# Performance work log

Hardware: AMD Instinct MI355X
Metric: run time of the kernel (lower is better)

## Reference

```python
import jax, jax.numpy as jnp
import numpy as np
from jax import lax

B, H, W = 256, 26, 4
LAT, QOUT = 64, 1024
K, D, Z = 4, 32, 64   # num_flows, num_ortho_vecs, z_size
STEPS = 100
BN_EPS = 1e-5


def setup_inputs():
    ks = iter(jax.random.split(jax.random.key(0), 80))
    def rn(shape, s=0.05):
        return jax.random.normal(next(ks), shape, jnp.float32) * s
    z1 = lambda n: jnp.zeros((n,), jnp.float32)
    o1 = lambda n: jnp.ones((n,), jnp.float32)
    return {
        "x": jax.random.normal(next(ks), (B, 1, H, W), jnp.float32),
        "eps": jax.random.normal(next(ks), (B, LAT), jnp.float32),
        "cw1": rn((32, 1, 3, 4)), "cb1": z1(32), "g1": o1(32), "be1": z1(32),
        "cw2": rn((16, 32, 5, 1)), "cb2": z1(16), "g2": o1(16), "be2": z1(16),
        "cw3": rn((8, 16, 7, 1)), "cb3": z1(8), "g3": o1(8), "be3": z1(8),
        "d1_w": rn((112, QOUT)), "d1_b": z1(QOUT), "bn1_g": o1(QOUT), "bn1_b": z1(QOUT),
        "mu_w": rn((QOUT, LAT)), "mu_b": z1(LAT),
        "lv_w": rn((QOUT, LAT)), "lv_b": z1(LAT),
        "ad_w": rn((QOUT, K * D * D)), "ad_b": z1(K * D * D),
        "adg1_w": rn((QOUT, K * D)), "adg1_b": z1(K * D),
        "adg2_w": rn((QOUT, K * D)), "adg2_b": z1(K * D),
        "aq_w": rn((QOUT, K * Z * D)), "aq_b": rn((K * Z * D,), 0.05),
        "ab_w": rn((QOUT, K * D)), "ab_b": z1(K * D),
        "d3_w": rn((LAT, QOUT)), "d3_b": z1(QOUT), "bn3_g": o1(QOUT), "bn3_b": z1(QOUT),
        "d4_w": rn((QOUT, 112)), "d4_b": z1(112), "bn4_g": o1(112), "bn4_b": z1(112),
        "tw1": rn((8, 16, 7, 1)), "tb1": z1(16), "tg1": o1(16), "tbe1": z1(16),
        "tw2": rn((16, 32, 5, 1)), "tb2": z1(32), "tg2": o1(32), "tbe2": z1(32),
        "tw3": rn((32, 1, 3, 4)), "tb3": z1(1),
    }


def _conv(x, w, b):
    y = lax.conv_general_dilated(x, w, (1, 1), 'VALID',
                                 dimension_numbers=('NCHW', 'OIHW', 'NCHW'))
    return y + b[None, :, None, None]


def _tconv(x, w, b):
    # torch ConvTranspose2d weight layout (in, out, kH, kW) == OIHW of the
    # forward conv being transposed -> transpose_kernel=True matches torch.
    y = lax.conv_transpose(x, w, (1, 1), 'VALID',
                           dimension_numbers=('NCHW', 'OIHW', 'NCHW'),
                           transpose_kernel=True)
    return y + b[None, :, None, None]


def _bn2d(x, g, b):  # BatchNorm2d, training mode (biased batch stats)
    m = x.mean((0, 2, 3), keepdims=True)
    v = ((x - m) ** 2).mean((0, 2, 3), keepdims=True)
    return (x - m) * lax.rsqrt(v + BN_EPS) * g[None, :, None, None] + b[None, :, None, None]


def _bn1d(x, g, b):  # BatchNorm1d, training mode
    m = x.mean(0)
    v = ((x - m) ** 2).mean(0)
    return (x - m) * lax.rsqrt(v + BN_EPS) * g + b


def reference(x, eps, cw1, cb1, g1, be1, cw2, cb2, g2, be2, cw3, cb3, g3, be3,
              d1_w, d1_b, bn1_g, bn1_b, mu_w, mu_b, lv_w, lv_b,
              ad_w, ad_b, adg1_w, adg1_b, adg2_w, adg2_b, aq_w, aq_b, ab_w, ab_b,
              d3_w, d3_b, bn3_g, bn3_b, d4_w, d4_b, bn4_g, bn4_b,
              tw1, tb1, tg1, tbe1, tw2, tb2, tg2, tbe2, tw3, tb3):
    # ---- encoder CNN ----
    h = jax.nn.relu(_bn2d(_conv(x, cw1, cb1), g1, be1))
    h = jax.nn.relu(_bn2d(_conv(h, cw2, cb2), g2, be2))
    h = jax.nn.relu(_bn2d(_conv(h, cw3, cb3), g3, be3))   # (B,8,14,1)
    out = h.reshape(B, -1)                                 # (B,112)
    out = jax.nn.relu(_bn1d(out @ d1_w + d1_b, bn1_g, bn1_b))
    mean = out @ mu_w + mu_b
    logvar = out @ lv_w + lv_b
    # ---- amortized flow parameters ----
    full_d = (out @ ad_w + ad_b).reshape(B, D, D, K)
    diag1 = jnp.tanh(out @ adg1_w + adg1_b).reshape(B, D, K)
    diag2 = jnp.tanh(out @ adg2_w + adg2_b).reshape(B, D, K)
    triu = jnp.triu(jnp.ones((D, D), x.dtype), 1)[None, :, :, None]
    di = jnp.arange(D)
    r1 = (full_d * triu).at[:, di, di, :].set(diag1)
    r2 = (jnp.transpose(full_d, (0, 2, 1, 3)) * triu).at[:, di, di, :].set(diag2)
    q = out @ aq_w + aq_b                                  # (B, K*Z*D)
    bflow = (out @ ab_w + ab_b).reshape(B, 1, D, K)
    # ---- Bjorck orthogonalization (100 fixed-point steps) ----
    qn = q.reshape(B * K, Z * D)
    qn = qn / jnp.linalg.norm(qn, axis=1, keepdims=True)
    amat = qn.reshape(B * K, Z, D)
    eye = jnp.eye(D, dtype=x.dtype)
    @jax.checkpoint
    def step(a, _):
        gram = jnp.einsum('nzd,nze->nde', a, a)            # a^T a, (N,D,D)
        a = jnp.einsum('nzd,nde->nze', a, eye + 0.5 * (eye - gram))
        return a, None
    amat, _ = lax.scan(step, amat, None, length=STEPS)
    q_ortho = amat.reshape(B, K, Z, D).transpose(1, 0, 2, 3)  # (K,B,Z,D)
    # ---- reparameterize + Sylvester flows ----
    z0 = mean + eps * jnp.exp(0.5 * logvar)
    z = z0
    ldj = jnp.zeros((B,), x.dtype)
    for k in range(K):
        r1k, r2k, qk, bk = r1[..., k], r2[..., k], q_ortho[k], bflow[..., k]
        qr2 = jnp.einsum('bzd,bed->bze', qk, r2k)          # q @ r2^T (B,Z,D)
        qr1 = jnp.einsum('bzd,bde->bze', qk, r1k)          # q @ r1   (B,Z,D)
        r2qzb = jnp.einsum('bz,bzd->bd', z, qr2)[:, None, :] + bk  # (B,1,D)
        z = jnp.einsum('bod,bzd->boz', jnp.tanh(r2qzb), qr1)[:, 0, :] + z
        dr1 = r1k[:, di, di]
        dr2 = r2k[:, di, di]
        diag_j = (1.0 - jnp.tanh(r2qzb) ** 2)[:, 0, :] * (dr1 * dr2) + 1.0
        ldj = ldj + jnp.log(jnp.abs(diag_j)).sum(-1)
    # ---- decoder ----
    d = jax.nn.relu(_bn1d(z @ d3_w + d3_b, bn3_g, bn3_b))
    d = jax.nn.relu(_bn1d(d @ d4_w + d4_b, bn4_g, bn4_b))
    d = d.reshape(B, 8, 14, 1)
    d = jax.nn.relu(_bn2d(_tconv(d, tw1, tb1), tg1, tbe1))
    d = jax.nn.relu(_bn2d(_tconv(d, tw2, tb2), tg2, tbe2))
    x_dec = _tconv(d, tw3, tb3)
    return (x_dec, mean, logvar, ldj, z0, z)
```

## Files before the change

### kernel.cpp

```cpp
#include <hip/hip_runtime.h>
#include <math.h>

#define NS_STEPS 30

typedef __attribute__((ext_vector_type(8))) _Float16 half8;
typedef __attribute__((ext_vector_type(4))) _Float16 half4v;
typedef __attribute__((ext_vector_type(8))) short short8;
typedef __attribute__((ext_vector_type(4))) float floatx4;

static __device__ inline unsigned short f2bf(float f) {
  union { float f; unsigned u; } v; v.f = f;
  unsigned r = v.u + 0x7fffu + ((v.u >> 16) & 1u);
  return (unsigned short)(r >> 16);
}
static __device__ inline float bf2f(unsigned short h) {
  union { unsigned u; float f; } v; v.u = ((unsigned)h) << 16;
  return v.f;
}

__global__ __launch_bounds__(256) void conv1_k(const float* __restrict__ x,
    const float* __restrict__ w, const float* __restrict__ bias,
    float* __restrict__ out) {
  __shared__ float ws[384];
  int tid = threadIdx.x;
  for (int i = tid; i < 384; i += 256) ws[i] = w[i];
  __syncthreads();
  int idx = blockIdx.x * 256 + tid;
  if (idx >= 196608) return;
  int b = idx / 768, r = idx % 768;
  int c = r / 24, h = r % 24;
  const float* xb = x + b * 104 + h * 4;
  const float* wc = ws + c * 12;
  float acc = bias[c];
  #pragma unroll
  for (int kh = 0; kh < 3; kh++) {
    #pragma unroll
    for (int kw = 0; kw < 4; kw++)
      acc += xb[kh * 4 + kw] * wc[kh * 4 + kw];
  }
  out[idx] = acc;
}

__global__ __launch_bounds__(256) void conv2_k(const float* __restrict__ in,
    const float* __restrict__ w, const float* __restrict__ bias,
    float* __restrict__ out) {
  __shared__ float ws[2560];
  int tid = threadIdx.x;
  for (int i = tid; i < 2560; i += 256) ws[i] = w[i];
  __syncthreads();
  int idx = blockIdx.x * 256 + tid;
  if (idx >= 81920) return;
  int b = idx / 320, r = idx % 320;
  int c = r / 20, h = r % 20;
  const float* ib = in + b * 768 + h;
  const float* wc = ws + c * 160;
  float acc = bias[c];
  for (int i = 0; i < 32; i++) {
    #pragma unroll
    for (int kh = 0; kh < 5; kh++)
      acc += ib[i * 24 + kh] * wc[i * 5 + kh];
  }
  out[idx] = acc;
}

__global__ __launch_bounds__(256) void conv3_k(const float* __restrict__ in,
    const float* __restrict__ w, const float* __restrict__ bias,
    float* __restrict__ out) {
  __shared__ float ws[896];
  int tid = threadIdx.x;
  for (int i = tid; i < 896; i += 256) ws[i] = w[i];
  __syncthreads();
  int idx = blockIdx.x * 256 + tid;
  if (idx >= 28672) return;
  int b = idx / 112, r = idx % 112;
  int c = r / 14, h = r % 14;
  const float* ib = in + b * 320 + h;
  const float* wc = ws + c * 112;
  float acc = bias[c];
  for (int i = 0; i < 16; i++) {
    #pragma unroll
    for (int kh = 0; kh < 7; kh++)
      acc += ib[i * 20 + kh] * wc[i * 7 + kh];
  }
  out[idx] = acc;
}

__global__ __launch_bounds__(256) void tconv1_k(const float* __restrict__ in,
    const float* __restrict__ w, const float* __restrict__ bias,
    float* __restrict__ out) {
  __shared__ float ws[896];
  int tid = threadIdx.x;
  for (int i = tid; i < 896; i += 256) ws[i] = w[i];
  __syncthreads();
  int idx = blockIdx.x * 256 + tid;
  if (idx >= 81920) return;
  int b = idx / 320, r = idx % 320;
  int c = r / 20, s = r % 20;
  float acc = bias[c];
  for (int o = 0; o < 8; o++) {
    #pragma unroll
    for (int kh = 0; kh < 7; kh++) {
      int hs = s - kh;
      if (hs >= 0 && hs < 14)
        acc += in[b * 112 + o * 14 + hs] * ws[o * 112 + c * 7 + kh];
    }
  }
  out[idx] = acc;
}

__global__ __launch_bounds__(256) void tconv2_k(const float* __restrict__ in,
    const float* __restrict__ w, const float* __restrict__ bias,
    float* __restrict__ out) {
  __shared__ float ws[2560];
  int tid = threadIdx.x;
  for (int i = tid; i < 2560; i += 256) ws[i] = w[i];
  __syncthreads();
  int idx = blockIdx.x * 256 + tid;
  if (idx >= 196608) return;
  int b = idx / 768, r = idx % 768;
  int c = r / 24, s = r % 24;
  float acc = bias[c];
  for (int o = 0; o < 16; o++) {
    #pragma unroll
    for (int kh = 0; kh < 5; kh++) {
      int hs = s - kh;
      if (hs >= 0 && hs < 20)
        acc += in[b * 320 + o * 20 + hs] * ws[o * 160 + c * 5 + kh];
    }
  }
  out[idx] = acc;
}

__global__ __launch_bounds__(256) void tconv3_k(const float* __restrict__ in,
    const float* __restrict__ w, const float* __restrict__ bias,
    float* __restrict__ out) {
  __shared__ float ws[384];
  int tid = threadIdx.x;
  for (int i = tid; i < 384; i += 256) ws[i] = w[i];
  __syncthreads();
  int idx = blockIdx.x * 256 + tid;
  if (idx >= 26624) return;
  int b = idx / 104, r = idx % 104;
  int sh = r / 4, sw = r % 4;
  float acc = bias[0];
  for (int o = 0; o < 32; o++) {
    #pragma unroll
    for (int kh = 0; kh < 3; kh++) {
      int hs = sh - kh;
      if (hs >= 0 && hs < 24)
        acc += in[b * 768 + o * 24 + hs] * ws[o * 12 + kh * 4 + sw];
    }
  }
  out[idx] = acc;
}

__global__ __launch_bounds__(256) void bn2d_k(float* __restrict__ x,
    const float* __restrict__ g, const float* __restrict__ be,
    int C, int HW) {
  __shared__ float rs[256], rs2[256];
  int c = blockIdx.x, tid = threadIdx.x;
  int total = 256 * HW;
  float s = 0.f, s2 = 0.f;
  for (int i = tid; i < total; i += 256) {
    int b = i / HW, j = i - b * HW;
    float v = x[(b * C + c) * HW + j];
    s += v; s2 += v * v;
  }
  rs[tid] = s; rs2[tid] = s2;
  __syncthreads();
  for (int off = 128; off > 0; off >>= 1) {
    if (tid < off) { rs[tid] += rs[tid + off]; rs2[tid] += rs2[tid + off]; }
    __syncthreads();
  }
  float m = rs[0] / (float)total;
  float var = rs2[0] / (float)total - m * m;
  float rstd = rsqrtf(var + 1e-5f) * g[c];
  float bb = be[c];
  for (int i = tid; i < total; i += 256) {
    int b = i / HW, j = i - b * HW;
    size_t idx = (size_t)(b * C + c) * HW + j;
    float v = (x[idx] - m) * rstd + bb;
    x[idx] = v > 0.f ? v : 0.f;
  }
}

__global__ __launch_bounds__(256) void bn1d_k(float* __restrict__ x,
    const float* __restrict__ g, const float* __restrict__ be, int N) {
  __shared__ float p1[8][32], p2[8][32];
  int t = threadIdx.x;
  int cl = t & 31, rg = t >> 5;
  int c = blockIdx.x * 32 + cl;
  float s = 0.f, s2 = 0.f;
  if (c < N) {
    for (int r = rg * 32; r < rg * 32 + 32; r++) {
      float v = x[r * N + c];
      s += v; s2 += v * v;
    }
  }
  p1[rg][cl] = s; p2[rg][cl] = s2;
  __syncthreads();
  float ts = 0.f, ts2 = 0.f;
  #pragma unroll
  for (int i = 0; i < 8; i++) { ts += p1[i][cl]; ts2 += p2[i][cl]; }
  float m = ts * (1.f / 256.f);
  float var = ts2 * (1.f / 256.f) - m * m;
  float rstd = rsqrtf(var + 1e-5f) * ((c < N) ? g[c] : 1.f);
  float bb = (c < N) ? be[c] : 0.f;
  if (c < N) {
    for (int r = rg * 32; r < rg * 32 + 32; r++) {
      float v = (x[r * N + c] - m) * rstd + bb;
      x[r * N + c] = v > 0.f ? v : 0.f;
    }
  }
}

__global__ __launch_bounds__(256) void gemm_os_k(const float* __restrict__ A,
    const float* __restrict__ W, const float* __restrict__ bias,
    float* __restrict__ C, int K, int N) {
  __shared__ float As[112 * 68];
  __shared__ float Bs[112 * 68];
  int tid = threadIdx.x;
  int nb = blockIdx.x, mb = blockIdx.y;
  int K16 = K >> 4;
  {
    int row = tid >> 2;
    const float* Ar = A + (size_t)(mb * 64 + row) * K;
    for (int i = 0; i < K16; i++) {
      int j = (tid & 3) + 4 * i;
      float4 v = *(const float4*)(Ar + j * 4);
      int k = j * 4;
      As[k * 68 + row] = v.x;
      As[(k + 1) * 68 + row] = v.y;
      As[(k + 2) * 68 + row] = v.z;
      As[(k + 3) * 68 + row] = v.w;
    }
  }
  {
    int n4 = (tid & 15) * 4;
    for (int i = 0; i < K16; i++) {
      int k = (tid >> 4) + 16 * i;
      float4 v = *(const float4*)(W + (size_t)k * N + nb * 64 + n4);
      *(float4*)(Bs + k * 68 + n4) = v;
    }
  }
  __syncthreads();
  int tm = tid >> 4, tn = tid & 15;
  int m0 = tm * 4, n0 = tn * 4;
  float acc[4][4] = {{0.f}};
  #pragma unroll 8
  for (int kk = 0; kk < K; kk++) {
    float4 a = *(const float4*)(As + kk * 68 + m0);
    float4 b = *(const float4*)(Bs + kk * 68 + n0);
    acc[0][0] += a.x*b.x; acc[0][1] += a.x*b.y; acc[0][2] += a.x*b.z; acc[0][3] += a.x*b.w;
    acc[1][0] += a.y*b.x; acc[1][1] += a.y*b.y; acc[1][2] += a.y*b.z; acc[1][3] += a.y*b.w;
    acc[2][0] += a.z*b.x; acc[2][1] += a.z*b.y; acc[2][2] += a.z*b.z; acc[2][3] += a.z*b.w;
    acc[3][0] += a.w*b.x; acc[3][1] += a.w*b.y; acc[3][2] += a.w*b.z; acc[3][3] += a.w*b.w;
  }
  #pragma unroll
  for (int i = 0; i < 4; i++) {
    int m = mb * 64 + m0 + i;
    #pragma unroll
    for (int j = 0; j < 4; j++) {
      int n = nb * 64 + n0 + j;
      C[(size_t)m * N + n] = acc[i][j] + bias[n];
    }
  }
}

__global__ __launch_bounds__(256) void gemm_ks_k(const float* __restrict__ A,
    const float* __restrict__ W, const float* __restrict__ bias,
    float* __restrict__ C) {
  __shared__ float As[64 * 68];
  __shared__ float Bs[64 * 68];
  int tid = threadIdx.x;
  int nb = blockIdx.x, mb = blockIdx.y, kc = blockIdx.z;
  int k0 = kc * 64;
  {
    int row = tid >> 2;
    const float* Ar = A + (size_t)(mb * 64 + row) * 1024 + k0;
    #pragma unroll
    for (int i = 0; i < 4; i++) {
      int j = (tid & 3) + 4 * i;
      float4 v = *(const float4*)(Ar + j * 4);
      int k = j * 4;
      As[k * 68 + row] = v.x;
      As[(k + 1) * 68 + row] = v.y;
      As[(k + 2) * 68 + row] = v.z;
      As[(k + 3) * 68 + row] = v.w;
    }
  }
  {
    int n4 = (tid & 15) * 4;
    int nbase = nb * 64 + n4;
    #pragma unroll
    for (int i = 0; i < 4; i++) {
      int k = (tid >> 4) + 16 * i;
      const float* Wr = W + (size_t)(k0 + k) * 112;
      float4 v;
      v.x = (nbase     < 112) ? Wr[nbase]     : 0.f;
      v.y = (nbase + 1 < 112) ? Wr[nbase + 1] : 0.f;
      v.z = (nbase + 2 < 112) ? Wr[nbase + 2] : 0.f;
      v.w = (nbase + 3 < 112) ? Wr[nbase + 3] : 0.f;
      *(float4*)(Bs + k * 68 + n4) = v;
    }
  }
  __syncthreads();
  int tm = tid >> 4, tn = tid & 15;
  int m0 = tm * 4, n0 = tn * 4;
  float acc[4][4] = {{0.f}};
  #pragma unroll 8
  for (int kk = 0; kk < 64; kk++) {
    float4 a = *(const float4*)(As + kk * 68 + m0);
    float4 b = *(const float4*)(Bs + kk * 68 + n0);
    acc[0][0] += a.x*b.x; acc[0][1] += a.x*b.y; acc[0][2] += a.x*b.z; acc[0][3] += a.x*b.w;
    acc[1][0] += a.y*b.x; acc[1][1] += a.y*b.y; acc[1][2] += a.y*b.z; acc[1][3] += a.y*b.w;
    acc[2][0] += a.z*b.x; acc[2][1] += a.z*b.y; acc[2][2] += a.z*b.z; acc[2][3] += a.z*b.w;
    acc[3][0] += a.w*b.x; acc[3][1] += a.w*b.y; acc[3][2] += a.w*b.z; acc[3][3] += a.w*b.w;
  }
  #pragma unroll
  for (int i = 0; i < 4; i++) {
    int m = mb * 64 + m0 + i;
    #pragma unroll
    for (int j = 0; j < 4; j++) {
      int n = nb * 64 + n0 + j;
      if (n < 112) {
        float v = acc[i][j] + (kc == 0 ? bias[n] : 0.f);
        atomicAdd(&C[m * 112 + n], v);
      }
    }
  }
}

__global__ __launch_bounds__(256) void prep_a_k(const float* __restrict__ A,
    short* __restrict__ ahi, short* __restrict__ alo) {
  int gi = blockIdx.x * 256 + threadIdx.x;
  int lane = gi & 63;
  int t = gi >> 6;
  int mt = t & 3; t >>= 2;
  int c = t & 31; int mb = t >> 5;
  int row = mb * 64 + mt * 16 + (lane & 15);
  int k0 = c * 32 + (lane >> 4) * 8;
  const float* src = A + (size_t)row * 1024 + k0;
  float4 v0 = *(const float4*)(src);
  float4 v1 = *(const float4*)(src + 4);
  float av[8] = {v0.x, v0.y, v0.z, v0.w, v1.x, v1.y, v1.z, v1.w};
  short8 h, lo;
  #pragma unroll
  for (int i = 0; i < 8; i++) {
    unsigned short hh = f2bf(av[i]);
    h[i] = (short)hh;
    lo[i] = (short)f2bf(av[i] - bf2f(hh));
  }
  *(short8*)(ahi + (size_t)gi * 8) = h;
  *(short8*)(alo + (size_t)gi * 8) = lo;
}

struct HeadArgs {
  const float* W[7];
  const float* b[7];
  float* dst[7];
  int off[8];
  int ldw[7];
  int op[7];
};

__global__ __launch_bounds__(256) void heads_mfma_k(const short* __restrict__ ahi,
                                                    const short* __restrict__ alo,
                                                    HeadArgs ha) {
  __shared__ __align__(16) short Wsh[2][2][2048];
  int tid = threadIdx.x;
  int nb = blockIdx.x;
  int r = 0;
  int gc = nb * 64;
  while (gc >= ha.off[r + 1]) r++;
  const float* Wp = ha.W[r];
  const float* bias = ha.b[r];
  float* dst = ha.dst[r];
  int ldw = ha.ldw[r];
  int op = ha.op[r];
  int nloc0 = gc - ha.off[r];

  int w = tid >> 6, l = tid & 63;
  int lane16 = l & 15, quad = l >> 4;

  int c64 = tid & 63, q4 = tid >> 6;
  const float* wcol = Wp + (size_t)q4 * 8 * ldw + nloc0 + c64;
  int wg = ((c64 >> 4) * 64 + q4 * 16 + (c64 & 15)) * 8;

  const short* agh = ahi + (size_t)w * 65536;
  const short* agl = alo + (size_t)w * 65536;

  const floatx4 zero4 = {0.f, 0.f, 0.f, 0.f};
  floatx4 acc[4][4];
  #pragma unroll
  for (int mt = 0; mt < 4; mt++)
    #pragma unroll
    for (int nf = 0; nf < 4; nf++) acc[mt][nf] = zero4;

  float wreg[8];
  short8 whi, wlo;
  short8 aCh[4], aCl[4], aNh[4], aNl[4];

  #pragma unroll
  for (int j = 0; j < 8; j++) wreg[j] = wcol[(size_t)j * ldw];
  #pragma unroll
  for (int j = 0; j < 8; j++) {
    unsigned short hh = f2bf(wreg[j]);
    whi[j] = (short)hh;
    wlo[j] = (short)f2bf(wreg[j] - bf2f(hh));
  }
  *(short8*)(&Wsh[0][0][wg]) = whi;
  *(short8*)(&Wsh[0][1][wg]) = wlo;
  #pragma unroll
  for (int j = 0; j < 8; j++) wreg[j] = wcol[(size_t)(32 + j) * ldw];
  #pragma unroll
  for (int mt = 0; mt < 4; mt++) {
    size_t ao = (size_t)mt * 512 + l * 8;
    aCh[mt] = *(const short8*)(agh + ao);
    aCl[mt] = *(const short8*)(agl + ao);
  }
  __syncthreads();
  #pragma unroll
  for (int j = 0; j < 8; j++) {
    unsigned short hh = f2bf(wreg[j]);
    whi[j] = (short)hh;
    wlo[j] = (short)f2bf(wreg[j] - bf2f(hh));
  }

  #pragma unroll 2
  for (int ch = 0; ch < 32; ++ch) {
    int p = ch & 1;
    if (ch < 31) {
      *(short8*)(&Wsh[p ^ 1][0][wg]) = whi;
      *(short8*)(&Wsh[p ^ 1][1][wg]) = wlo;
    }
    if (ch < 30) {
      #pragma unroll
      for (int j = 0; j < 8; j++)
        wreg[j] = wcol[(size_t)((ch + 2) * 32 + j) * ldw];
    }
    if (ch < 31) {
      #pragma unroll
      for (int mt = 0; mt < 4; mt++) {
        size_t ao = (size_t)((ch + 1) * 4 + mt) * 512 + l * 8;
        aNh[mt] = *(const short8*)(agh + ao);
        aNl[mt] = *(const short8*)(agl + ao);
      }
    }
    short8 bh[4], bl[4];
    #pragma unroll
    for (int nf = 0; nf < 4; nf++) {
      bh[nf] = *(const short8*)(&Wsh[p][0][(nf * 64 + l) * 8]);
      bl[nf] = *(const short8*)(&Wsh[p][1][(nf * 64 + l) * 8]);
    }
    #pragma unroll
    for (int mt = 0; mt < 4; mt++)
      #pragma unroll
      for (int nf = 0; nf < 4; nf++) {
        acc[mt][nf] = __builtin_amdgcn_mfma_f32_16x16x32_bf16(aCh[mt], bh[nf], acc[mt][nf], 0, 0, 0);
        acc[mt][nf] = __builtin_amdgcn_mfma_f32_16x16x32_bf16(aCh[mt], bl[nf], acc[mt][nf], 0, 0, 0);
        acc[mt][nf] = __builtin_amdgcn_mfma_f32_16x16x32_bf16(aCl[mt], bh[nf], acc[mt][nf], 0, 0, 0);
      }
    if (ch < 30) {
      #pragma unroll
      for (int j = 0; j < 8; j++) {
        unsigned short hh = f2bf(wreg[j]);
        whi[j] = (short)hh;
        wlo[j] = (short)f2bf(wreg[j] - bf2f(hh));
      }
    }
    if (ch < 31) {
      #pragma unroll
      for (int mt = 0; mt < 4; mt++) { aCh[mt] = aNh[mt]; aCl[mt] = aNl[mt]; }
    }
    __syncthreads();
  }

  #pragma unroll
  for (int nf = 0; nf < 4; nf++) {
    int n = nloc0 + nf * 16 + lane16;
    float bv = bias[n];
    #pragma unroll
    for (int mt = 0; mt < 4; mt++) {
      #pragma unroll
      for (int i = 0; i < 4; i++) {
        int m = w * 64 + mt * 16 + quad * 4 + i;
        float v = acc[mt][nf][i] + bv;
        if (op == 1) v = tanhf(v);
        dst[(size_t)m * ldw + n] = v;
      }
    }
  }
}

__global__ __launch_bounds__(64) void ns_f16split_k(const float* __restrict__ q,
                                                    float* __restrict__ amat) {
  __align__(16) __shared__ _Float16 arena[12288];
  int l = threadIdx.x;
  int lane16 = l & 15, quad = l >> 4;
  _Float16* Ah_cm = arena;
  _Float16* Al_cm = arena + 2304;
  _Float16* Mh_cm = arena + 4608;
  _Float16* Ml_cm = arena + 5888;
  _Float16* Ah_rm = arena + 7168;
  _Float16* Al_rm = arena + 9728;
  float* Afin = (float*)arena;

  const float* g = q + (size_t)blockIdx.x * 2048;
  float* o = amat + (size_t)blockIdx.x * 2048;

  float vals[32];
  float ss = 0.f;
  #pragma unroll
  for (int j = 0; j < 8; j++) {
    float4 v = *(const float4*)(g + l * 32 + j * 4);
    vals[4*j] = v.x; vals[4*j+1] = v.y; vals[4*j+2] = v.z; vals[4*j+3] = v.w;
    ss += v.x*v.x + v.y*v.y + v.z*v.z + v.w*v.w;
  }
  #pragma unroll
  for (int off = 32; off > 0; off >>= 1) ss += __shfl_xor(ss, off);
  float rn = rsqrtf(ss);
  #pragma unroll
  for (int i = 0; i < 32; i++) vals[i] *= rn;
  #pragma unroll
  for (int j = 0; j < 8; j++) {
    half4v ph, pl;
    #pragma unroll
    for (int r = 0; r < 4; r++) {
      float v = vals[4*j + r];
      _Float16 h = (_Float16)v;
      _Float16 lo = (_Float16)(v - (float)h);
      ph[r] = h; pl[r] = lo;
    }
    *(half4v*)(Ah_rm + l * 40 + j * 4) = ph;
    *(half4v*)(Al_rm + l * 40 + j * 4) = pl;
  }
  #pragma unroll
  for (int i = 0; i < 32; i++) {
    float v = vals[i];
    _Float16 h = (_Float16)v;
    Ah_cm[i * 72 + l] = h;
    Al_cm[i * 72 + l] = (_Float16)(v - (float)h);
  }
  __syncthreads();

  const floatx4 zero4 = {0.f, 0.f, 0.f, 0.f};
  for (int s = 0; s < NS_STEPS; s++) {
    bool last = (s == NS_STEPS - 1);
    half8 fah[2][2], fal[2][2];
    #pragma unroll
    for (int ti = 0; ti < 2; ti++)
      #pragma unroll
      for (int c = 0; c < 2; c++) {
        fah[ti][c] = *(half8*)(Ah_cm + (ti * 16 + lane16) * 72 + c * 32 + quad * 8);
        fal[ti][c] = *(half8*)(Al_cm + (ti * 16 + lane16) * 72 + c * 32 + quad * 8);
      }
    floatx4 gf[2][2] = {{zero4, zero4}, {zero4, zero4}};
    #pragma unroll
    for (int ti = 0; ti < 2; ti++)
      #pragma unroll
      for (int tj = 0; tj < 2; tj++)
        #pragma unroll
        for (int c = 0; c < 2; c++) {
          gf[ti][tj] = __builtin_amdgcn_mfma_f32_16x16x32_f16(
              fah[ti][c], fah[tj][c], gf[ti][tj], 0, 0, 0);
          gf[ti][tj] = __builtin_amdgcn_mfma_f32_16x16x32_f16(
              fah[ti][c], fal[tj][c], gf[ti][tj], 0, 0, 0);
          gf[ti][tj] = __builtin_amdgcn_mfma_f32_16x16x32_f16(
              fal[ti][c], fah[tj][c], gf[ti][tj], 0, 0, 0);
        }
    #pragma unroll
    for (int ti = 0; ti < 2; ti++)
      #pragma unroll
      for (int tj = 0; tj < 2; tj++) {
        int col = tj * 16 + lane16;
        int row0 = ti * 16 + quad * 4;
        half4v ph, pl;
        #pragma unroll
        for (int r = 0; r < 4; r++) {
          float m = ((row0 + r) == col ? 1.5f : 0.f) - 0.5f * gf[ti][tj][r];
          _Float16 h = (_Float16)m;
          ph[r] = h; pl[r] = (_Float16)(m - (float)h);
        }
        *(half4v*)(Mh_cm + col * 40 + row0) = ph;
        *(half4v*)(Ml_cm + col * 40 + row0) = pl;
      }
    __syncthreads();
    half8 fmh[2], fml[2], fbh[4], fbl[4];
    #pragma unroll
    for (int ti = 0; ti < 2; ti++) {
      fmh[ti] = *(half8*)(Mh_cm + (ti * 16 + lane16) * 40 + quad * 8);
      fml[ti] = *(half8*)(Ml_cm + (ti * 16 + lane16) * 40 + quad * 8);
    }
    #pragma unroll
    for (int tj = 0; tj < 4; tj++) {
      fbh[tj] = *(half8*)(Ah_rm + (tj * 16 + lane16) * 40 + quad * 8);
      fbl[tj] = *(half8*)(Al_rm + (tj * 16 + lane16) * 40 + quad * 8);
    }
    floatx4 df[2][4];
    #pragma unroll
    for (int ti = 0; ti < 2; ti++)
      #pragma unroll
      for (int tj = 0; tj < 4; tj++) {
        df[ti][tj] = __builtin_amdgcn_mfma_f32_16x16x32_f16(
            fmh[ti], fbh[tj], zero4, 0, 0, 0);
        df[ti][tj] = __builtin_amdgcn_mfma_f32_16x16x32_f16(
            fmh[ti], fbl[tj], df[ti][tj], 0, 0, 0);
        df[ti][tj] = __builtin_amdgcn_mfma_f32_16x16x32_f16(
            fml[ti], fbh[tj], df[ti][tj], 0, 0, 0);
      }
    __syncthreads();
    if (!last) {
      #pragma unroll
      for (int ti = 0; ti < 2; ti++)
        #pragma unroll
        for (int tj = 0; tj < 4; tj++) {
          int z = tj * 16 + lane16;
          int d0 = ti * 16 + quad * 4;
          half4v ph, pl;
          #pragma unroll
          for (int r = 0; r < 4; r++) {
            float v = df[ti][tj][r];
            _Float16 h = (_Float16)v;
            ph[r] = h; pl[r] = (_Float16)(v - (float)h);
          }
          *(half4v*)(Ah_rm + z * 40 + d0) = ph;
          *(half4v*)(Al_rm + z * 40 + d0) = pl;
          #pragma unroll
          for (int r = 0; r < 4; r++) {
            Ah_cm[(d0 + r) * 72 + z] = ph[r];
            Al_cm[(d0 + r) * 72 + z] = pl[r];
          }
        }
    } else {
      #pragma unroll
      for (int ti = 0; ti < 2; ti++)
        #pragma unroll
        for (int tj = 0; tj < 4; tj++) {
          int z = tj * 16 + lane16;
          int d0 = ti * 16 + quad * 4;
          float4 v;
          v.x = df[ti][tj][0]; v.y = df[ti][tj][1];
          v.z = df[ti][tj][2]; v.w = df[ti][tj][3];
          *(float4*)(Afin + z * 36 + d0) = v;
        }
    }
    __syncthreads();
  }
  #pragma unroll
  for (int j = 0; j < 8; j++) {
    int f = j * 256 + l * 4;
    int z = f >> 5, d = f & 31;
    float4 v = *(const float4*)(Afin + z * 36 + d);
    *(float4*)(o + f) = v;
  }
}

__global__ __launch_bounds__(64) void flow_k(const float* __restrict__ amat,
    const float* __restrict__ fd, const float* __restrict__ dg1,
    const float* __restrict__ dg2, const float* __restrict__ ab,
    const float* __restrict__ eps, float* __restrict__ dout) {
  __shared__ float Ps[32][64];
  __shared__ float wsh[32], tsh[32], ush[32];
  int b = blockIdx.x, l = threadIdx.x;
  float mv  = dout[26624 + b * 64 + l];
  float lvv = dout[43008 + b * 64 + l];
  float z0 = mv + eps[b * 64 + l] * expf(0.5f * lvv);
  dout[59648 + b * 64 + l] = z0;
  float zv = z0;
  float ldj = 0.f;
  float q[32];
  for (int k = 0; k < 4; k++) {
    const float4* qrow = (const float4*)(amat + (size_t)(b * 4 + k) * 2048 + l * 32);
    #pragma unroll
    for (int j = 0; j < 8; j++) {
      float4 v = qrow[j];
      q[4*j] = v.x; q[4*j+1] = v.y; q[4*j+2] = v.z; q[4*j+3] = v.w;
    }
    #pragma unroll
    for (int d = 0; d < 32; d++) Ps[d][l] = zv * q[d];
    __syncthreads();
    if (l < 32) {
      const float4* pr = (const float4*)Ps[l];
      float s = 0.f;
      #pragma unroll
      for (int j = 0; j < 16; j++) {
        float4 v = pr[j];
        s += v.x + v.y + v.z + v.w;
      }
      wsh[l] = s;
    }
    __syncthreads();
    if (l < 32) {
      int e = l;
      float acc = ab[b * 128 + e * 4 + k] + wsh[e] * dg2[b * 128 + e * 4 + k];
      for (int d = e + 1; d < 32; d++)
        acc += wsh[d] * fd[b * 4096 + d * 128 + e * 4 + k];
      float tt = tanhf(acc);
      tsh[e] = tt;
      float dd = (1.f - tt * tt) * (dg1[b*128 + e*4 + k] * dg2[b*128 + e*4 + k]) + 1.f;
      ldj += logf(fabsf(dd));
    }
    __syncthreads();
    if (l < 32) {
      int d = l;
      float acc = tsh[d] * dg1[b * 128 + d * 4 + k];
      for (int e = d + 1; e < 32; e++)
        acc += fd[b * 4096 + d * 128 + e * 4 + k] * tsh[e];
      ush[d] = acc;
    }
    __syncthreads();
    #pragma unroll
    for (int d = 0; d < 32; d++) zv += q[d] * ush[d];
    __syncthreads();
  }
  dout[76032 + b * 64 + l] = zv;
  for (int off = 16; off > 0; off >>= 1) ldj += __shfl_down(ldj, off, 32);
  if (l == 0) dout[59392 + b] = ldj;
}

extern "C" void kernel_launch(void* const* d_in, const int* in_sizes, int n_in,
                              void* d_out, int out_size, void* d_ws, size_t ws_size,
                              hipStream_t stream) {
  (void)in_sizes; (void)n_in; (void)out_size; (void)ws_size;
  const float* x     = (const float*)d_in[0];
  const float* eps   = (const float*)d_in[1];
  const float* cw1   = (const float*)d_in[2];
  const float* cb1   = (const float*)d_in[3];
  const float* g1    = (const float*)d_in[4];
  const float* be1   = (const float*)d_in[5];
  const float* cw2   = (const float*)d_in[6];
  const float* cb2   = (const float*)d_in[7];
  const float* g2    = (const float*)d_in[8];
  const float* be2   = (const float*)d_in[9];
  const float* cw3   = (const float*)d_in[10];
  const float* cb3   = (const float*)d_in[11];
  const float* g3    = (const float*)d_in[12];
  const float* be3   = (const float*)d_in[13];
  const float* d1_w  = (const float*)d_in[14];
  const float* d1_b  = (const float*)d_in[15];
  const float* bn1_g = (const float*)d_in[16];
  const float* bn1_b = (const float*)d_in[17];
  const float* mu_w  = (const float*)d_in[18];
  const float* mu_b  = (const float*)d_in[19];
  const float* lv_w  = (const float*)d_in[20];
  const float* lv_b  = (const float*)d_in[21];
  const float* ad_w  = (const float*)d_in[22];
  const float* ad_b  = (const float*)d_in[23];
  const float* adg1_w= (const float*)d_in[24];
  const float* adg1_b= (const float*)d_in[25];
  const float* adg2_w= (const float*)d_in[26];
  const float* adg2_b= (const float*)d_in[27];
  const float* aq_w  = (const float*)d_in[28];
  const float* aq_b  = (const float*)d_in[29];
  const float* ab_w  = (const float*)d_in[30];
  const float* ab_b  = (const float*)d_in[31];
  const float* d3_w  = (const float*)d_in[32];
  const float* d3_b  = (const float*)d_in[33];
  const float* bn3_g = (const float*)d_in[34];
  const float* bn3_b = (const float*)d_in[35];
  const float* d4_w  = (const float*)d_in[36];
  const float* d4_b  = (const float*)d_in[37];
  const float* bn4_g = (const float*)d_in[38];
  const float* bn4_b = (const float*)d_in[39];
  const float* tw1   = (const float*)d_in[40];
  const float* tb1   = (const float*)d_in[41];
  const float* tg1   = (const float*)d_in[42];
  const float* tbe1  = (const float*)d_in[43];
  const float* tw2   = (const float*)d_in[44];
  const float* tb2   = (const float*)d_in[45];
  const float* tg2   = (const float*)d_in[46];
  const float* tbe2  = (const float*)d_in[47];
  const float* tw3   = (const float*)d_in[48];
  const float* tb3   = (const float*)d_in[49];

  float* out = (float*)d_out;
  float* wsf = (float*)d_ws;
  float* h1   = wsf;
  float* h2   = wsf + 196608;
  float* h3   = wsf + 278528;
  float* out1 = wsf + 307200;
  float* fd   = wsf + 569344;
  float* dg1  = wsf + 1617920;
  float* dg2  = wsf + 1650688;
  float* qb   = wsf + 1683456;
  float* ab   = wsf + 3780608;
  float* amat = wsf + 3813376;
  float* dec1 = out1;
  float* dec2 = h3;
  float* t1   = h2;
  float* t2   = h1;

  short* ahi = (short*)wsf;
  short* alo = ahi + 262144;

  float* mean_o = out + 26624;
  float* lv_o   = out + 43008;
  float* z_o    = out + 76032;

  conv1_k<<<768, 256, 0, stream>>>(x, cw1, cb1, h1);
  bn2d_k<<<32, 256, 0, stream>>>(h1, g1, be1, 32, 24);
  conv2_k<<<320, 256, 0, stream>>>(h1, cw2, cb2, h2);
  bn2d_k<<<16, 256, 0, stream>>>(h2, g2, be2, 16, 20);
  conv3_k<<<112, 256, 0, stream>>>(h2, cw3, cb3, h3);
  bn2d_k<<<8, 256, 0, stream>>>(h3, g3, be3, 8, 14);

  gemm_os_k<<<dim3(16, 4), 256, 0, stream>>>(h3, d1_w, d1_b, out1, 112, 1024);
  bn1d_k<<<32, 256, 0, stream>>>(out1, bn1_g, bn1_b, 1024);

  prep_a_k<<<128, 256, 0, stream>>>(out1, ahi, alo);

  HeadArgs ha;
  ha.W[0] = mu_w;   ha.b[0] = mu_b;   ha.dst[0] = mean_o; ha.ldw[0] = 64;   ha.op[0] = 0;
  ha.W[1] = lv_w;   ha.b[1] = lv_b;   ha.dst[1] = lv_o;   ha.ldw[1] = 64;   ha.op[1] = 0;
  ha.W[2] = ad_w;   ha.b[2] = ad_b;   ha.dst[2] = fd;     ha.ldw[2] = 4096; ha.op[2] = 0;
  ha.W[3] = adg1_w; ha.b[3] = adg1_b; ha.dst[3] = dg1;    ha.ldw[3] = 128;  ha.op[3] = 1;
  ha.W[4] = adg2_w; ha.b[4] = adg2_b; ha.dst[4] = dg2;    ha.ldw[4] = 128;  ha.op[4] = 1;
  ha.W[5] = aq_w;   ha.b[5] = aq_b;   ha.dst[5] = qb;     ha.ldw[5] = 8192; ha.op[5] = 0;
  ha.W[6] = ab_w;   ha.b[6] = ab_b;   ha.dst[6] = ab;     ha.ldw[6] = 128;  ha.op[6] = 0;
  ha.off[0] = 0;    ha.off[1] = 64;   ha.off[2] = 128;  ha.off[3] = 4224;
  ha.off[4] = 4352; ha.off[5] = 4480; ha.off[6] = 12672; ha.off[7] = 12800;
  heads_mfma_k<<<dim3(200), 256, 0, stream>>>(ahi, alo, ha);

  ns_f16split_k<<<1024, 64, 0, stream>>>(qb, amat);
  flow_k<<<256, 64, 0, stream>>>(amat, fd, dg1, dg2, ab, eps, out);

  gemm_os_k<<<dim3(16, 4), 256, 0, stream>>>(z_o, d3_w, d3_b, dec1, 64, 1024);
  bn1d_k<<<32, 256, 0, stream>>>(dec1, bn3_g, bn3_b, 1024);
  hipMemsetAsync(dec2, 0, 28672 * sizeof(float), stream);
  gemm_ks_k<<<dim3(2, 4, 16), 256, 0, stream>>>(dec1, d4_w, d4_b, dec2);
  bn1d_k<<<4, 256, 0, stream>>>(dec2, bn4_g, bn4_b, 112);

  tconv1_k<<<320, 256, 0, stream>>>(dec2, tw1, tb1, t1);
  bn2d_k<<<16, 256, 0, stream>>>(t1, tg1, tbe1, 16, 20);
  tconv2_k<<<768, 256, 0, stream>>>(t1, tw2, tb2, t2);
  bn2d_k<<<32, 256, 0, stream>>>(t2, tg2, tbe2, 32, 24);
  tconv3_k<<<104, 256, 0, stream>>>(t2, tw3, tb3, out);
}
```

Baseline: 521.8 us.

## Narrow heads GEMM tiles to 16 columns and split Newton-Schulz across two waves

The heads GEMM now gives each block 16 output columns instead of 64, launching 800 blocks instead of 200. Each lane loads its own weight fragment straight into registers, so the shared-memory staging and barriers go away. The Newton-Schulz orthogonalisation kernel moves from one wave to two per block, with each wave computing half of the Gram and update tiles. The aim is more parallelism and occupancy on a 256-CU part, at the cost of re-reading the activation operands four times more often in the heads GEMM and uncoalesced, strided weight loads.

```diff
diff --git a/kernel.cpp b/kernel.cpp
--- a/kernel.cpp
+++ b/kernel.cpp
@@ -367,77 +367,57 @@
 __global__ __launch_bounds__(256) void heads_mfma_k(const short* __restrict__ ahi,
                                                     const short* __restrict__ alo,
                                                     HeadArgs ha) {
-  __shared__ __align__(16) short Wsh[2][2][2048];
   int tid = threadIdx.x;
   int nb = blockIdx.x;
+  int gc = nb * 16;
   int r = 0;
-  int gc = nb * 64;
   while (gc >= ha.off[r + 1]) r++;
   const float* Wp = ha.W[r];
   const float* bias = ha.b[r];
   float* dst = ha.dst[r];
   int ldw = ha.ldw[r];
   int op = ha.op[r];
-  int nloc0 = gc - ha.off[r];
+  int nloc = gc - ha.off[r];
 
   int w = tid >> 6, l = tid & 63;
   int lane16 = l & 15, quad = l >> 4;
 
-  int c64 = tid & 63, q4 = tid >> 6;
-  const float* wcol = Wp + (size_t)q4 * 8 * ldw + nloc0 + c64;
-  int wg = ((c64 >> 4) * 64 + q4 * 16 + (c64 & 15)) * 8;
-
+  const float* wptr = Wp + (size_t)(quad * 8) * ldw + nloc + lane16;
   const short* agh = ahi + (size_t)w * 65536;
   const short* agl = alo + (size_t)w * 65536;
 
   const floatx4 zero4 = {0.f, 0.f, 0.f, 0.f};
-  floatx4 acc[4][4];
-  #pragma unroll
-  for (int mt = 0; mt < 4; mt++)
-    #pragma unroll
-    for (int nf = 0; nf < 4; nf++) acc[mt][nf] = zero4;
-
-  float wreg[8];
+  floatx4 acc[4] = {zero4, zero4, zero4, zero4};
+
+  float wvN[8], wvF[8];
   short8 whi, wlo;
   short8 aCh[4], aCl[4], aNh[4], aNl[4];
 
-  #pragma unroll
-  for (int j = 0; j < 8; j++) wreg[j] = wcol[(size_t)j * ldw];
-  #pragma unroll
-  for (int j = 0; j < 8; j++) {
-    unsigned short hh = f2bf(wreg[j]);
-    whi[j] = (short)hh;
-    wlo[j] = (short)f2bf(wreg[j] - bf2f(hh));
-  }
-  *(short8*)(&Wsh[0][0][wg]) = whi;
-  *(short8*)(&Wsh[0][1][wg]) = wlo;
-  #pragma unroll
-  for (int j = 0; j < 8; j++) wreg[j] = wcol[(size_t)(32 + j) * ldw];
-  #pragma unroll
-  for (int mt = 0; mt < 4; mt++) {
-    size_t ao = (size_t)mt * 512 + l * 8;
-    aCh[mt] = *(const short8*)(agh + ao);
-    aCl[mt] = *(const short8*)(agl + ao);
-  }
-  __syncthreads();
-  #pragma unroll
-  for (int j = 0; j < 8; j++) {
-    unsigned short hh = f2bf(wreg[j]);
-    whi[j] = (short)hh;
-    wlo[j] = (short)f2bf(wreg[j] - bf2f(hh));
-  }
-
-  #pragma unroll 2
+  {
+    float wv0[8];
+    #pragma unroll
+    for (int j = 0; j < 8; j++) wv0[j] = wptr[(size_t)j * ldw];
+    #pragma unroll
+    for (int mt = 0; mt < 4; mt++) {
+      size_t ao = (size_t)mt * 512 + l * 8;
+      aCh[mt] = *(const short8*)(agh + ao);
+      aCl[mt] = *(const short8*)(agl + ao);
+    }
+    #pragma unroll
+    for (int j = 0; j < 8; j++) wvN[j] = wptr[(size_t)(32 + j) * ldw];
+    #pragma unroll
+    for (int j = 0; j < 8; j++) {
+      unsigned short hh = f2bf(wv0[j]);
+      whi[j] = (short)hh;
+      wlo[j] = (short)f2bf(wv0[j] - bf2f(hh));
+    }
+  }
+
   for (int ch = 0; ch < 32; ++ch) {
-    int p = ch & 1;
-    if (ch < 31) {
-      *(short8*)(&Wsh[p ^ 1][0][wg]) = whi;
-      *(short8*)(&Wsh[p ^ 1][1][wg]) = wlo;
-    }
     if (ch < 30) {
       #pragma unroll
       for (int j = 0; j < 8; j++)
-        wreg[j] = wcol[(size_t)((ch + 2) * 32 + j) * ldw];
+        wvF[j] = wptr[(size_t)((ch + 2) * 32 + j) * ldw];
     }
     if (ch < 31) {
       #pragma unroll
@@ -447,56 +427,48 @@
         aNl[mt] = *(const short8*)(agl + ao);
       }
     }
-    short8 bh[4], bl[4];
-    #pragma unroll
-    for (int nf = 0; nf < 4; nf++) {
-      bh[nf] = *(const short8*)(&Wsh[p][0][(nf * 64 + l) * 8]);
-      bl[nf] = *(const short8*)(&Wsh[p][1][(nf * 64 + l) * 8]);
-    }
-    #pragma unroll
-    for (int mt = 0; mt < 4; mt++)
-      #pragma unroll
-      for (int nf = 0; nf < 4; nf++) {
-        acc[mt][nf] = __builtin_amdgcn_mfma_f32_16x16x32_bf16(aCh[mt], bh[nf], acc[mt][nf], 0, 0, 0);
-        acc[mt][nf] = __builtin_amdgcn_mfma_f32_16x16x32_bf16(aCh[mt], bl[nf], acc[mt][nf], 0, 0, 0);
-        acc[mt][nf] = __builtin_amdgcn_mfma_f32_16x16x32_bf16(aCl[mt], bh[nf], acc[mt][nf], 0, 0, 0);
+    #pragma unroll
+    for (int mt = 0; mt < 4; mt++) {
+      acc[mt] = __builtin_amdgcn_mfma_f32_16x16x32_bf16(aCh[mt], whi, acc[mt], 0, 0, 0);
+      acc[mt] = __builtin_amdgcn_mfma_f32_16x16x32_bf16(aCh[mt], wlo, acc[mt], 0, 0, 0);
+      acc[mt] = __builtin_amdgcn_mfma_f32_16x16x32_bf16(aCl[mt], whi, acc[mt], 0, 0, 0);
+    }
+    if (ch < 31) {
+      #pragma unroll
+      for (int j = 0; j < 8; j++) {
+        unsigned short hh = f2bf(wvN[j]);
+        whi[j] = (short)hh;
+        wlo[j] = (short)f2bf(wvN[j] - bf2f(hh));
       }
+      #pragma unroll
+      for (int mt = 0; mt < 4; mt++) { aCh[mt] = aNh[mt]; aCl[mt] = aNl[mt]; }
+    }
     if (ch < 30) {
       #pragma unroll
-      for (int j = 0; j < 8; j++) {
-        unsigned short hh = f2bf(wreg[j]);
-        whi[j] = (short)hh;
-        wlo[j] = (short)f2bf(wreg[j] - bf2f(hh));
-      }
-    }
-    if (ch < 31) {
-      #pragma unroll
-      for (int mt = 0; mt < 4; mt++) { aCh[mt] = aNh[mt]; aCl[mt] = aNl[mt]; }
-    }
-    __syncthreads();
-  }
-
+      for (int j = 0; j < 8; j++) wvN[j] = wvF[j];
+    }
+  }
+
+  int n = nloc + lane16;
+  float bv = bias[n];
   #pragma unroll
-  for (int nf = 0; nf < 4; nf++) {
-    int n = nloc0 + nf * 16 + lane16;
-    float bv = bias[n];
-    #pragma unroll
-    for (int mt = 0; mt < 4; mt++) {
-      #pragma unroll
-      for (int i = 0; i < 4; i++) {
-        int m = w * 64 + mt * 16 + quad * 4 + i;
-        float v = acc[mt][nf][i] + bv;
-        if (op == 1) v = tanhf(v);
-        dst[(size_t)m * ldw + n] = v;
-      }
-    }
-  }
-}
-
-__global__ __launch_bounds__(64) void ns_f16split_k(const float* __restrict__ q,
-                                                    float* __restrict__ amat) {
+  for (int mt = 0; mt < 4; mt++) {
+    #pragma unroll
+    for (int i = 0; i < 4; i++) {
+      int m = w * 64 + mt * 16 + quad * 4 + i;
+      float v = acc[mt][i] + bv;
+      if (op == 1) v = tanhf(v);
+      dst[(size_t)m * ldw + n] = v;
+    }
+  }
+}
+
+__global__ __launch_bounds__(128) void ns_f16split_k(const float* __restrict__ q,
+                                                     float* __restrict__ amat) {
   __align__(16) __shared__ _Float16 arena[12288];
-  int l = threadIdx.x;
+  int tid = threadIdx.x;
+  int wid = tid >> 6;
+  int l = tid & 63;
   int lane16 = l & 15, quad = l >> 4;
   _Float16* Ah_cm = arena;
   _Float16* Al_cm = arena + 2304;
@@ -509,38 +481,40 @@
   const float* g = q + (size_t)blockIdx.x * 2048;
   float* o = amat + (size_t)blockIdx.x * 2048;
 
-  float vals[32];
-  float ss = 0.f;
-  #pragma unroll
-  for (int j = 0; j < 8; j++) {
-    float4 v = *(const float4*)(g + l * 32 + j * 4);
-    vals[4*j] = v.x; vals[4*j+1] = v.y; vals[4*j+2] = v.z; vals[4*j+3] = v.w;
-    ss += v.x*v.x + v.y*v.y + v.z*v.z + v.w*v.w;
-  }
-  #pragma unroll
-  for (int off = 32; off > 0; off >>= 1) ss += __shfl_xor(ss, off);
-  float rn = rsqrtf(ss);
-  #pragma unroll
-  for (int i = 0; i < 32; i++) vals[i] *= rn;
-  #pragma unroll
-  for (int j = 0; j < 8; j++) {
-    half4v ph, pl;
-    #pragma unroll
-    for (int r = 0; r < 4; r++) {
-      float v = vals[4*j + r];
+  if (wid == 0) {
+    float vals[32];
+    float ss = 0.f;
+    #pragma unroll
+    for (int j = 0; j < 8; j++) {
+      float4 v = *(const float4*)(g + l * 32 + j * 4);
+      vals[4*j] = v.x; vals[4*j+1] = v.y; vals[4*j+2] = v.z; vals[4*j+3] = v.w;
+      ss += v.x*v.x + v.y*v.y + v.z*v.z + v.w*v.w;
+    }
+    #pragma unroll
+    for (int off = 32; off > 0; off >>= 1) ss += __shfl_xor(ss, off);
+    float rn = rsqrtf(ss);
+    #pragma unroll
+    for (int i = 0; i < 32; i++) vals[i] *= rn;
+    #pragma unroll
+    for (int j = 0; j < 8; j++) {
+      half4v ph, pl;
+      #pragma unroll
+      for (int rr = 0; rr < 4; rr++) {
+        float v = vals[4*j + rr];
+        _Float16 h = (_Float16)v;
+        _Float16 lo = (_Float16)(v - (float)h);
+        ph[rr] = h; pl[rr] = lo;
+      }
+      *(half4v*)(Ah_rm + l * 40 + j * 4) = ph;
+      *(half4v*)(Al_rm + l * 40 + j * 4) = pl;
+    }
+    #pragma unroll
+    for (int i = 0; i < 32; i++) {
+      float v = vals[i];
       _Float16 h = (_Float16)v;
-      _Float16 lo = (_Float16)(v - (float)h);
-      ph[r] = h; pl[r] = lo;
-    }
-    *(half4v*)(Ah_rm + l * 40 + j * 4) = ph;
-    *(half4v*)(Al_rm + l * 40 + j * 4) = pl;
-  }
-  #pragma unroll
-  for (int i = 0; i < 32; i++) {
-    float v = vals[i];
-    _Float16 h = (_Float16)v;
-    Ah_cm[i * 72 + l] = h;
-    Al_cm[i * 72 + l] = (_Float16)(v - (float)h);
+      Ah_cm[i * 72 + l] = h;
+      Al_cm[i * 72 + l] = (_Float16)(v - (float)h);
+    }
   }
   __syncthreads();
 
@@ -555,101 +529,100 @@
         fah[ti][c] = *(half8*)(Ah_cm + (ti * 16 + lane16) * 72 + c * 32 + quad * 8);
         fal[ti][c] = *(half8*)(Al_cm + (ti * 16 + lane16) * 72 + c * 32 + quad * 8);
       }
-    floatx4 gf[2][2] = {{zero4, zero4}, {zero4, zero4}};
+    floatx4 gf[2] = {zero4, zero4};
     #pragma unroll
     for (int ti = 0; ti < 2; ti++)
       #pragma unroll
-      for (int tj = 0; tj < 2; tj++)
-        #pragma unroll
-        for (int c = 0; c < 2; c++) {
-          gf[ti][tj] = __builtin_amdgcn_mfma_f32_16x16x32_f16(
-              fah[ti][c], fah[tj][c], gf[ti][tj], 0, 0, 0);
-          gf[ti][tj] = __builtin_amdgcn_mfma_f32_16x16x32_f16(
-              fah[ti][c], fal[tj][c], gf[ti][tj], 0, 0, 0);
-          gf[ti][tj] = __builtin_amdgcn_mfma_f32_16x16x32_f16(
-              fal[ti][c], fah[tj][c], gf[ti][tj], 0, 0, 0);
-        }
-    #pragma unroll
-    for (int ti = 0; ti < 2; ti++)
-      #pragma unroll
-      for (int tj = 0; tj < 2; tj++) {
-        int col = tj * 16 + lane16;
-        int row0 = ti * 16 + quad * 4;
-        half4v ph, pl;
-        #pragma unroll
-        for (int r = 0; r < 4; r++) {
-          float m = ((row0 + r) == col ? 1.5f : 0.f) - 0.5f * gf[ti][tj][r];
-          _Float16 h = (_Float16)m;
-          ph[r] = h; pl[r] = (_Float16)(m - (float)h);
-        }
-        *(half4v*)(Mh_cm + col * 40 + row0) = ph;
-        *(half4v*)(Ml_cm + col * 40 + row0) = pl;
+      for (int c = 0; c < 2; c++) {
+        gf[ti] = __builtin_amdgcn_mfma_f32_16x16x32_f16(
+            fah[ti][c], fah[wid][c], gf[ti], 0, 0, 0);
+        gf[ti] = __builtin_amdgcn_mfma_f32_16x16x32_f16(
+            fah[ti][c], fal[wid][c], gf[ti], 0, 0, 0);
+        gf[ti] = __builtin_amdgcn_mfma_f32_16x16x32_f16(
+            fal[ti][c], fah[wid][c], gf[ti], 0, 0, 0);
       }
+    #pragma unroll
+    for (int ti = 0; ti < 2; ti++) {
+      int col = wid * 16 + lane16;
+      int row0 = ti * 16 + quad * 4;
+      half4v ph, pl;
+      #pragma unroll
+      for (int rr = 0; rr < 4; rr++) {
+        float m = ((row0 + rr) == col ? 1.5f : 0.f) - 0.5f * gf[ti][rr];
+        _Float16 h = (_Float16)m;
+        ph[rr] = h; pl[rr] = (_Float16)(m - (float)h);
+      }
+      *(half4v*)(Mh_cm + col * 40 + row0) = ph;
+      *(half4v*)(Ml_cm + col * 40 + row0) = pl;
+    }
     __syncthreads();
-    half8 fmh[2], fml[2], fbh[4], fbl[4];
+    half8 fmh[2], fml[2], fbh[2], fbl[2];
     #pragma unroll
     for (int ti = 0; ti < 2; ti++) {
       fmh[ti] = *(half8*)(Mh_cm + (ti * 16 + lane16) * 40 + quad * 8);
       fml[ti] = *(half8*)(Ml_cm + (ti * 16 + lane16) * 40 + quad * 8);
     }
     #pragma unroll
-    for (int tj = 0; tj < 4; tj++) {
-      fbh[tj] = *(half8*)(Ah_rm + (tj * 16 + lane16) * 40 + quad * 8);
-      fbl[tj] = *(half8*)(Al_rm + (tj * 16 + lane16) * 40 + quad * 8);
-    }
-    floatx4 df[2][4];
+    for (int jj = 0; jj < 2; jj++) {
+      int tj = 2 * wid + jj;
+      fbh[jj] = *(half8*)(Ah_rm + (tj * 16 + lane16) * 40 + quad * 8);
+      fbl[jj] = *(half8*)(Al_rm + (tj * 16 + lane16) * 40 + quad * 8);
+    }
+    floatx4 df[2][2];
     #pragma unroll
     for (int ti = 0; ti < 2; ti++)
       #pragma unroll
-      for (int tj = 0; tj < 4; tj++) {
-        df[ti][tj] = __builtin_amdgcn_mfma_f32_16x16x32_f16(
-            fmh[ti], fbh[tj], zero4, 0, 0, 0);
-        df[ti][tj] = __builtin_amdgcn_mfma_f32_16x16x32_f16(
-            fmh[ti], fbl[tj], df[ti][tj], 0, 0, 0);
-        df[ti][tj] = __builtin_amdgcn_mfma_f32_16x16x32_f16(
-            fml[ti], fbh[tj], df[ti][tj], 0, 0, 0);
+      for (int jj = 0; jj < 2; jj++) {
+        df[ti][jj] = __builtin_amdgcn_mfma_f32_16x16x32_f16(
+            fmh[ti], fbh[jj], zero4, 0, 0, 0);
+        df[ti][jj] = __builtin_amdgcn_mfma_f32_16x16x32_f16(
+            fmh[ti], fbl[jj], df[ti][jj], 0, 0, 0);
+        df[ti][jj] = __builtin_amdgcn_mfma_f32_16x16x32_f16(
+            fml[ti], fbh[jj], df[ti][jj], 0, 0, 0);
       }
     __syncthreads();
     if (!last) {
       #pragma unroll
       for (int ti = 0; ti < 2; ti++)
         #pragma unroll
-        for (int tj = 0; tj < 4; tj++) {
+        for (int jj = 0; jj < 2; jj++) {
+          int tj = 2 * wid + jj;
           int z = tj * 16 + lane16;
           int d0 = ti * 16 + quad * 4;
           half4v ph, pl;
           #pragma unroll
-          for (int r = 0; r < 4; r++) {
-            float v = df[ti][tj][r];
+          for (int rr = 0; rr < 4; rr++) {
+            float v = df[ti][jj][rr];
             _Float16 h = (_Float16)v;
-            ph[r] = h; pl[r] = (_Float16)(v - (float)h);
+            ph[rr] = h; pl[rr] = (_Float16)(v - (float)h);
           }
           *(half4v*)(Ah_rm + z * 40 + d0) = ph;
           *(half4v*)(Al_rm + z * 40 + d0) = pl;
           #pragma unroll
-          for (int r = 0; r < 4; r++) {
-            Ah_cm[(d0 + r) * 72 + z] = ph[r];
-            Al_cm[(d0 + r) * 72 + z] = pl[r];
+          for (int rr = 0; rr < 4; rr++) {
+            Ah_cm[(d0 + rr) * 72 + z] = ph[rr];
+            Al_cm[(d0 + rr) * 72 + z] = pl[rr];
           }
         }
     } else {
       #pragma unroll
       for (int ti = 0; ti < 2; ti++)
         #pragma unroll
-        for (int tj = 0; tj < 4; tj++) {
+        for (int jj = 0; jj < 2; jj++) {
+          int tj = 2 * wid + jj;
           int z = tj * 16 + lane16;
           int d0 = ti * 16 + quad * 4;
           float4 v;
-          v.x = df[ti][tj][0]; v.y = df[ti][tj][1];
-          v.z = df[ti][tj][2]; v.w = df[ti][tj][3];
+          v.x = df[ti][jj][0]; v.y = df[ti][jj][1];
+          v.z = df[ti][jj][2]; v.w = df[ti][jj][3];
           *(float4*)(Afin + z * 36 + d0) = v;
         }
     }
     __syncthreads();
   }
   #pragma unroll
-  for (int j = 0; j < 8; j++) {
-    int f = j * 256 + l * 4;
+  for (int j = 0; j < 4; j++) {
+    int f = j * 512 + tid * 4;
     int z = f >> 5, d = f & 31;
     float4 v = *(const float4*)(Afin + z * 36 + d);
     *(float4*)(o + f) = v;
@@ -820,9 +793,9 @@
   ha.W[6] = ab_w;   ha.b[6] = ab_b;   ha.dst[6] = ab;     ha.ldw[6] = 128;  ha.op[6] = 0;
   ha.off[0] = 0;    ha.off[1] = 64;   ha.off[2] = 128;  ha.off[3] = 4224;
   ha.off[4] = 4352; ha.off[5] = 4480; ha.off[6] = 12672; ha.off[7] = 12800;
-  heads_mfma_k<<<dim3(200), 256, 0, stream>>>(ahi, alo, ha);
-
-  ns_f16split_k<<<1024, 64, 0, stream>>>(qb, amat);
+  heads_mfma_k<<<dim3(800), 256, 0, stream>>>(ahi, alo, ha);
+
+  ns_f16split_k<<<1024, 128, 0, stream>>>(qb, amat);
   flow_k<<<256, 64, 0, stream>>>(amat, fd, dg1, dg2, ab, eps, out);
 
   gemm_os_k<<<dim3(16, 4), 256, 0, stream>>>(z_o, d3_w, d3_b, dec1, 64, 1024);
```

New measurement: 752.1 us. +44.1%, slower.
